# Optimization experiments

Measured on AMD Instinct MI355X. Metric: run time of the kernel, lower is better.

The kernel has to match this reference:

```python
import jax, jax.numpy as jnp
import numpy as np

B, H, L, D = 8, 8, 2048, 64  # head_sz = d_model // h = 512 // 8

def setup_inputs() -> dict:
    key = jax.random.key(0)
    kq, kk, kv = jax.random.split(key, 3)
    Q = jax.random.normal(kq, (B, H, L, D), dtype=jnp.float32)
    K = jax.random.normal(kk, (B, H, L, D), dtype=jnp.float32)
    V = jax.random.normal(kv, (B, H, L, D), dtype=jnp.float32)
    return {"Q": Q, "K": K, "V": V}

def reference(Q, K, V):
    head_sz = Q.shape[-1]
    # NOTE: original code divides by torch.tensor([head_sz]) (raw head size, not sqrt)
    prod = jnp.einsum('bhld,bhmd->bhlm', Q, K) / head_sz  # [B,H,L,L]
    att = jax.nn.softmax(prod, axis=-1)
    # dropout is identity in eval mode (reference is deterministic)
    res = jnp.einsum('bhlm,bhmd->bhld', att, V)  # [B,H,L,D]
    return (res, att)
```

## Files before the change

kernel.cpp:

```cpp
#include <hip/hip_runtime.h>

#define NB 8
#define NH 8
#define LSEQ 2048
#define DH 64

typedef __attribute__((ext_vector_type(8))) short bf16x8;
typedef __attribute__((ext_vector_type(4))) short bf16x4v;
typedef __attribute__((ext_vector_type(4))) float f32x4;

__device__ __forceinline__ short f2bf(float f) {
    union { float f; unsigned u; } v; v.f = f;
    unsigned r = v.u + 0x7fffu + ((v.u >> 16) & 1u);
    return (short)(r >> 16);
}
__device__ __forceinline__ float bf2f(short s) {
    union { unsigned u; float f; } v;
    v.u = ((unsigned)(unsigned short)s) << 16;
    return v.f;
}

__global__ __launch_bounds__(256, 2)
void sdpa_kernel(const float* __restrict__ Q, const float* __restrict__ K,
                 const float* __restrict__ V, float* __restrict__ out_res,
                 float* __restrict__ out_att)
{
    __shared__ short P[16 * 2048];

    const int tid  = threadIdx.x;
    const int lane = tid & 63;
    const int w    = tid >> 6;
    const int q16  = lane & 15;
    const int quad = lane >> 4;

    const int bh    = blockIdx.x >> 7;
    const int qbase = (blockIdx.x & 127) << 4;

    const size_t qkv0 = (size_t)bh * (LSEQ * DH);

    bf16x8 aq0, aq1;
    {
        const float* qp = Q + qkv0 + (size_t)(qbase + q16) * DH + quad * 8;
        float4 f0 = *(const float4*)(qp);
        float4 f1 = *(const float4*)(qp + 4);
        float4 f2 = *(const float4*)(qp + 32);
        float4 f3 = *(const float4*)(qp + 36);
        aq0[0]=f2bf(f0.x); aq0[1]=f2bf(f0.y); aq0[2]=f2bf(f0.z); aq0[3]=f2bf(f0.w);
        aq0[4]=f2bf(f1.x); aq0[5]=f2bf(f1.y); aq0[6]=f2bf(f1.z); aq0[7]=f2bf(f1.w);
        aq1[0]=f2bf(f2.x); aq1[1]=f2bf(f2.y); aq1[2]=f2bf(f2.z); aq1[3]=f2bf(f2.w);
        aq1[4]=f2bf(f3.x); aq1[5]=f2bf(f3.y); aq1[6]=f2bf(f3.z); aq1[7]=f2bf(f3.w);
    }

    const int key_lo = w << 9;
    for (int t = 0; t < 32; ++t) {
        const int key0 = key_lo + (t << 4);
        const float* kp = K + qkv0 + (size_t)(key0 + q16) * DH + quad * 8;
        float4 f0 = *(const float4*)(kp);
        float4 f1 = *(const float4*)(kp + 4);
        float4 f2 = *(const float4*)(kp + 32);
        float4 f3 = *(const float4*)(kp + 36);
        bf16x8 b0, b1;
        b0[0]=f2bf(f0.x); b0[1]=f2bf(f0.y); b0[2]=f2bf(f0.z); b0[3]=f2bf(f0.w);
        b0[4]=f2bf(f1.x); b0[5]=f2bf(f1.y); b0[6]=f2bf(f1.z); b0[7]=f2bf(f1.w);
        b1[0]=f2bf(f2.x); b1[1]=f2bf(f2.y); b1[2]=f2bf(f2.z); b1[3]=f2bf(f2.w);
        b1[4]=f2bf(f3.x); b1[5]=f2bf(f3.y); b1[6]=f2bf(f3.z); b1[7]=f2bf(f3.w);
        f32x4 acc = {0.f, 0.f, 0.f, 0.f};
        acc = __builtin_amdgcn_mfma_f32_16x16x32_bf16(aq0, b0, acc, 0, 0, 0);
        acc = __builtin_amdgcn_mfma_f32_16x16x32_bf16(aq1, b1, acc, 0, 0, 0);
        const int col = key0 + q16;
        const int chb = col >> 3;
        const int off = col & 7;
        #pragma unroll
        for (int r = 0; r < 4; ++r) {
            const int row = (quad << 2) + r;
            const float p = __expf(acc[r] * 0.015625f);
            P[(row << 11) + (((chb ^ (row & 7)) << 3) + off)] = f2bf(p);
        }
    }
    __syncthreads();

    float s = 0.f;
    {
        const int rb2 = q16 << 11;
        const int x7  = q16 & 7;
        for (int c = 0; c < 64; ++c) {
            const int ch = (quad << 6) + c;
            const bf16x8 v = *(const bf16x8*)&P[rb2 + ((ch ^ x7) << 3)];
            #pragma unroll
            for (int j = 0; j < 8; ++j) s += bf2f(v[j]);
        }
    }
    s += __shfl_xor(s, 16, 64);
    s += __shfl_xor(s, 32, 64);
    const float linv_own = 1.0f / s;

    const int nb = w << 4;
    const float* vb = V + qkv0 + nb + q16;
    f32x4 accA = {0.f,0.f,0.f,0.f}, accB = {0.f,0.f,0.f,0.f};
    const int rbq = q16 << 11;
    const int x7q = q16 & 7;
    for (int it = 0; it < 32; ++it) {
        const int chA = (it << 2) + quad;
        const int chB = chA + 128;
        const bf16x8 aA = *(const bf16x8*)&P[rbq + ((chA ^ x7q) << 3)];
        const bf16x8 aB = *(const bf16x8*)&P[rbq + ((chB ^ x7q) << 3)];
        const float* vpA = vb + (size_t)((it << 5) + (quad << 3)) * DH;
        const float* vpB = vpA + (size_t)1024 * DH;
        bf16x8 bA, bB;
        #pragma unroll
        for (int j = 0; j < 8; ++j) bA[j] = f2bf(vpA[(size_t)j * DH]);
        #pragma unroll
        for (int j = 0; j < 8; ++j) bB[j] = f2bf(vpB[(size_t)j * DH]);
        accA = __builtin_amdgcn_mfma_f32_16x16x32_bf16(aA, bA, accA, 0, 0, 0);
        accB = __builtin_amdgcn_mfma_f32_16x16x32_bf16(aB, bB, accB, 0, 0, 0);
    }
    {
        float* orow = out_res + qkv0 + (size_t)qbase * DH + nb + q16;
        #pragma unroll
        for (int r = 0; r < 4; ++r) {
            const int row = (quad << 2) + r;
            const float li = __shfl(linv_own, row, 64);
            orow[(size_t)row * DH] = (accA[r] + accB[r]) * li;
        }
    }

    float* ab = out_att + ((size_t)bh * LSEQ + qbase) * LSEQ;
    for (int i = 0; i < 32; ++i) {
        const int idx = tid + (i << 8);
        const int row = idx >> 9;
        const int col = (idx & 511) << 2;
        const int ch  = col >> 3;
        const int off = col & 7;
        const float li = __shfl(linv_own, row, 64);
        const bf16x4v v = *(const bf16x4v*)&P[(row << 11) + ((ch ^ (row & 7)) << 3) + off];
        float4 o;
        o.x = bf2f(v[0]) * li;
        o.y = bf2f(v[1]) * li;
        o.z = bf2f(v[2]) * li;
        o.w = bf2f(v[3]) * li;
        *(float4*)(ab + (size_t)row * LSEQ + col) = o;
    }
}

extern "C" void kernel_launch(void* const* d_in, const int* in_sizes, int n_in,
                              void* d_out, int out_size, void* d_ws, size_t ws_size,
                              hipStream_t stream) {
    const float* Q = (const float*)d_in[0];
    const float* K = (const float*)d_in[1];
    const float* V = (const float*)d_in[2];
    float* out_res = (float*)d_out;
    float* out_att = out_res + (size_t)NB * NH * LSEQ * DH;
    dim3 grid(NB * NH * (LSEQ / 16));
    sdpa_kernel<<<grid, dim3(256), 0, stream>>>(Q, K, V, out_res, out_att);
}
```

Before: 2.029 ms.

## Split into bf16 pre-conversion, row-sum pass, and streaming fused attention pass

Pre-converts K to bf16 and transposes V to bf16 in workspace. A separate pass recomputes QK^T and exp to get softmax row sums. The main kernel then recomputes scores, normalizes them, streams the attention matrix with nontemporal stores and does P@V through a small LDS staging buffer. This removes the large per-block LDS buffer that limited occupancy and the strided fp32 V gathers, at the cost of computing QK^T twice and launching extra kernels.

After: 1.666 ms. -17.9%, faster.

```diff
diff --git a/kernel.cpp b/kernel.cpp
--- a/kernel.cpp
+++ b/kernel.cpp
@@ -4,9 +4,9 @@
 #define NH 8
 #define LSEQ 2048
 #define DH 64
+#define NBH (NB * NH)
 
 typedef __attribute__((ext_vector_type(8))) short bf16x8;
-typedef __attribute__((ext_vector_type(4))) short bf16x4v;
 typedef __attribute__((ext_vector_type(4))) float f32x4;
 
 __device__ __forceinline__ short f2bf(float f) {
@@ -14,131 +14,180 @@
     unsigned r = v.u + 0x7fffu + ((v.u >> 16) & 1u);
     return (short)(r >> 16);
 }
-__device__ __forceinline__ float bf2f(short s) {
-    union { unsigned u; float f; } v;
-    v.u = ((unsigned)(unsigned short)s) << 16;
-    return v.f;
-}
-
-__global__ __launch_bounds__(256, 2)
-void sdpa_kernel(const float* __restrict__ Q, const float* __restrict__ K,
-                 const float* __restrict__ V, float* __restrict__ out_res,
-                 float* __restrict__ out_att)
-{
-    __shared__ short P[16 * 2048];
-
-    const int tid  = threadIdx.x;
+
+__device__ __forceinline__ void load_q_frags(const float* __restrict__ qp,
+                                             bf16x8& a0, bf16x8& a1) {
+    float4 f0 = *(const float4*)(qp);
+    float4 f1 = *(const float4*)(qp + 4);
+    float4 f2 = *(const float4*)(qp + 32);
+    float4 f3 = *(const float4*)(qp + 36);
+    a0[0]=f2bf(f0.x); a0[1]=f2bf(f0.y); a0[2]=f2bf(f0.z); a0[3]=f2bf(f0.w);
+    a0[4]=f2bf(f1.x); a0[5]=f2bf(f1.y); a0[6]=f2bf(f1.z); a0[7]=f2bf(f1.w);
+    a1[0]=f2bf(f2.x); a1[1]=f2bf(f2.y); a1[2]=f2bf(f2.z); a1[3]=f2bf(f2.w);
+    a1[4]=f2bf(f3.x); a1[5]=f2bf(f3.y); a1[6]=f2bf(f3.z); a1[7]=f2bf(f3.w);
+}
+
+__global__ __launch_bounds__(256)
+void conv_k(const float* __restrict__ K, short* __restrict__ Kbf) {
+    const size_t i = ((size_t)blockIdx.x * 256 + threadIdx.x) * 8;
+    float4 f0 = *(const float4*)(K + i);
+    float4 f1 = *(const float4*)(K + i + 4);
+    bf16x8 o;
+    o[0]=f2bf(f0.x); o[1]=f2bf(f0.y); o[2]=f2bf(f0.z); o[3]=f2bf(f0.w);
+    o[4]=f2bf(f1.x); o[5]=f2bf(f1.y); o[6]=f2bf(f1.z); o[7]=f2bf(f1.w);
+    *(bf16x8*)(Kbf + i) = o;
+}
+
+__global__ __launch_bounds__(256)
+void transp_v(const float* __restrict__ V, short* __restrict__ Vt) {
+    __shared__ __align__(16) short t[DH][64];
+    const int tid = threadIdx.x;
+    const int bh = blockIdx.x >> 5;
+    const int l0 = (blockIdx.x & 31) << 6;
+    const float* vb = V + ((size_t)bh * LSEQ + l0) * DH;
+    #pragma unroll
+    for (int p = 0; p < 4; ++p) {
+        const int l = (p << 4) + (tid >> 4);
+        const int d0 = (tid & 15) << 2;
+        float4 f = *(const float4*)(vb + (size_t)l * DH + d0);
+        const int lc = l >> 3, li = l & 7;
+        const int g = d0 >> 3;
+        t[d0 + 0][((lc ^ g) << 3) + li] = f2bf(f.x);
+        t[d0 + 1][((lc ^ g) << 3) + li] = f2bf(f.y);
+        t[d0 + 2][((lc ^ g) << 3) + li] = f2bf(f.z);
+        t[d0 + 3][((lc ^ g) << 3) + li] = f2bf(f.w);
+    }
+    __syncthreads();
+    const int d = tid >> 2;
+    const int s2 = (tid & 3) << 1;
+    const int g = d >> 3;
+    short* ob = Vt + ((size_t)bh * DH + d) * LSEQ + l0 + (s2 << 3);
+    *(bf16x8*)(ob)     = *(const bf16x8*)&t[d][(s2 ^ g) << 3];
+    *(bf16x8*)(ob + 8) = *(const bf16x8*)&t[d][((s2 + 1) ^ g) << 3];
+}
+
+__global__ __launch_bounds__(256, 4)
+void rowsum_k(const float* __restrict__ Q, const short* __restrict__ Kbf,
+              float* __restrict__ rsum) {
+    const int tid = threadIdx.x;
     const int lane = tid & 63;
-    const int w    = tid >> 6;
-    const int q16  = lane & 15;
+    const int w = tid >> 6;
+    const int q16 = lane & 15;
     const int quad = lane >> 4;
-
-    const int bh    = blockIdx.x >> 7;
-    const int qbase = (blockIdx.x & 127) << 4;
-
+    const int nb_ = ((blockIdx.x & 7) << 8) + (blockIdx.x >> 3);
+    const int bh = nb_ >> 5;
+    const int qbase = ((nb_ & 31) << 6) + (w << 4);
     const size_t qkv0 = (size_t)bh * (LSEQ * DH);
 
     bf16x8 aq0, aq1;
+    load_q_frags(Q + qkv0 + (size_t)(qbase + q16) * DH + quad * 8, aq0, aq1);
+
+    float rs0 = 0.f, rs1 = 0.f, rs2 = 0.f, rs3 = 0.f;
+    const short* kb = Kbf + qkv0 + (size_t)q16 * DH + quad * 8;
+    for (int c = 0; c < 64; ++c) {
+        const short* kp = kb + (size_t)(c << 5) * DH;
+        bf16x8 b00 = *(const bf16x8*)(kp);
+        bf16x8 b01 = *(const bf16x8*)(kp + 32);
+        bf16x8 b10 = *(const bf16x8*)(kp + 16 * DH);
+        bf16x8 b11 = *(const bf16x8*)(kp + 16 * DH + 32);
+        f32x4 s0 = {0.f,0.f,0.f,0.f}, s1 = {0.f,0.f,0.f,0.f};
+        s0 = __builtin_amdgcn_mfma_f32_16x16x32_bf16(aq0, b00, s0, 0, 0, 0);
+        s0 = __builtin_amdgcn_mfma_f32_16x16x32_bf16(aq1, b01, s0, 0, 0, 0);
+        s1 = __builtin_amdgcn_mfma_f32_16x16x32_bf16(aq0, b10, s1, 0, 0, 0);
+        s1 = __builtin_amdgcn_mfma_f32_16x16x32_bf16(aq1, b11, s1, 0, 0, 0);
+        rs0 += __expf(s0[0] * 0.015625f) + __expf(s1[0] * 0.015625f);
+        rs1 += __expf(s0[1] * 0.015625f) + __expf(s1[1] * 0.015625f);
+        rs2 += __expf(s0[2] * 0.015625f) + __expf(s1[2] * 0.015625f);
+        rs3 += __expf(s0[3] * 0.015625f) + __expf(s1[3] * 0.015625f);
+    }
+    #pragma unroll
+    for (int m = 1; m < 16; m <<= 1) {
+        rs0 += __shfl_xor(rs0, m, 64);
+        rs1 += __shfl_xor(rs1, m, 64);
+        rs2 += __shfl_xor(rs2, m, 64);
+        rs3 += __shfl_xor(rs3, m, 64);
+    }
+    if (q16 == 0) {
+        float* rp = rsum + (size_t)bh * LSEQ + qbase + (quad << 2);
+        rp[0] = rs0; rp[1] = rs1; rp[2] = rs2; rp[3] = rs3;
+    }
+}
+
+__global__ __launch_bounds__(256, 4)
+void sdpa_main(const float* __restrict__ Q, const short* __restrict__ Kbf,
+               const short* __restrict__ Vt, const float* __restrict__ rsum,
+               float* __restrict__ out_res, float* __restrict__ out_att) {
+    __shared__ __align__(16) short pbuf[4][16][40];
+    const int tid = threadIdx.x;
+    const int lane = tid & 63;
+    const int w = tid >> 6;
+    const int q16 = lane & 15;
+    const int quad = lane >> 4;
+
+    const int nb_ = ((blockIdx.x & 7) << 8) + (blockIdx.x >> 3);
+    const int bh = nb_ >> 5;
+    const int qbase = ((nb_ & 31) << 6) + (w << 4);
+    const size_t qkv0 = (size_t)bh * (LSEQ * DH);
+
+    bf16x8 aq0, aq1;
+    load_q_frags(Q + qkv0 + (size_t)(qbase + q16) * DH + quad * 8, aq0, aq1);
+
+    float linv[4];
     {
-        const float* qp = Q + qkv0 + (size_t)(qbase + q16) * DH + quad * 8;
-        float4 f0 = *(const float4*)(qp);
-        float4 f1 = *(const float4*)(qp + 4);
-        float4 f2 = *(const float4*)(qp + 32);
-        float4 f3 = *(const float4*)(qp + 36);
-        aq0[0]=f2bf(f0.x); aq0[1]=f2bf(f0.y); aq0[2]=f2bf(f0.z); aq0[3]=f2bf(f0.w);
-        aq0[4]=f2bf(f1.x); aq0[5]=f2bf(f1.y); aq0[6]=f2bf(f1.z); aq0[7]=f2bf(f1.w);
-        aq1[0]=f2bf(f2.x); aq1[1]=f2bf(f2.y); aq1[2]=f2bf(f2.z); aq1[3]=f2bf(f2.w);
-        aq1[4]=f2bf(f3.x); aq1[5]=f2bf(f3.y); aq1[6]=f2bf(f3.z); aq1[7]=f2bf(f3.w);
-    }
-
-    const int key_lo = w << 9;
-    for (int t = 0; t < 32; ++t) {
-        const int key0 = key_lo + (t << 4);
-        const float* kp = K + qkv0 + (size_t)(key0 + q16) * DH + quad * 8;
-        float4 f0 = *(const float4*)(kp);
-        float4 f1 = *(const float4*)(kp + 4);
-        float4 f2 = *(const float4*)(kp + 32);
-        float4 f3 = *(const float4*)(kp + 36);
-        bf16x8 b0, b1;
-        b0[0]=f2bf(f0.x); b0[1]=f2bf(f0.y); b0[2]=f2bf(f0.z); b0[3]=f2bf(f0.w);
-        b0[4]=f2bf(f1.x); b0[5]=f2bf(f1.y); b0[6]=f2bf(f1.z); b0[7]=f2bf(f1.w);
-        b1[0]=f2bf(f2.x); b1[1]=f2bf(f2.y); b1[2]=f2bf(f2.z); b1[3]=f2bf(f2.w);
-        b1[4]=f2bf(f3.x); b1[5]=f2bf(f3.y); b1[6]=f2bf(f3.z); b1[7]=f2bf(f3.w);
-        f32x4 acc = {0.f, 0.f, 0.f, 0.f};
-        acc = __builtin_amdgcn_mfma_f32_16x16x32_bf16(aq0, b0, acc, 0, 0, 0);
-        acc = __builtin_amdgcn_mfma_f32_16x16x32_bf16(aq1, b1, acc, 0, 0, 0);
-        const int col = key0 + q16;
-        const int chb = col >> 3;
-        const int off = col & 7;
+        const float* rp = rsum + (size_t)bh * LSEQ + qbase + (quad << 2);
+        linv[0] = 1.0f / rp[0];
+        linv[1] = 1.0f / rp[1];
+        linv[2] = 1.0f / rp[2];
+        linv[3] = 1.0f / rp[3];
+    }
+
+    f32x4 acc0 = {0.f,0.f,0.f,0.f}, acc1 = {0.f,0.f,0.f,0.f};
+    f32x4 acc2 = {0.f,0.f,0.f,0.f}, acc3 = {0.f,0.f,0.f,0.f};
+
+    const short* kb = Kbf + qkv0 + (size_t)q16 * DH + quad * 8;
+    const short* vb = Vt + (size_t)bh * (DH * LSEQ) + (size_t)q16 * LSEQ + quad * 8;
+    float* ab = out_att + ((size_t)bh * LSEQ + qbase + (quad << 2)) * LSEQ + q16;
+    short* pw = &pbuf[w][quad << 2][q16];
+    const short* pr = &pbuf[w][q16][quad << 3];
+
+    for (int c = 0; c < 64; ++c) {
+        const int col0 = c << 5;
+        const short* kp = kb + (size_t)col0 * DH;
+        bf16x8 b00 = *(const bf16x8*)(kp);
+        bf16x8 b01 = *(const bf16x8*)(kp + 32);
+        bf16x8 b10 = *(const bf16x8*)(kp + 16 * DH);
+        bf16x8 b11 = *(const bf16x8*)(kp + 16 * DH + 32);
+        f32x4 s0 = {0.f,0.f,0.f,0.f}, s1 = {0.f,0.f,0.f,0.f};
+        s0 = __builtin_amdgcn_mfma_f32_16x16x32_bf16(aq0, b00, s0, 0, 0, 0);
+        s0 = __builtin_amdgcn_mfma_f32_16x16x32_bf16(aq1, b01, s0, 0, 0, 0);
+        s1 = __builtin_amdgcn_mfma_f32_16x16x32_bf16(aq0, b10, s1, 0, 0, 0);
+        s1 = __builtin_amdgcn_mfma_f32_16x16x32_bf16(aq1, b11, s1, 0, 0, 0);
+
         #pragma unroll
         for (int r = 0; r < 4; ++r) {
-            const int row = (quad << 2) + r;
-            const float p = __expf(acc[r] * 0.015625f);
-            P[(row << 11) + (((chb ^ (row & 7)) << 3) + off)] = f2bf(p);
+            const float p0 = __expf(s0[r] * 0.015625f) * linv[r];
+            const float p1 = __expf(s1[r] * 0.015625f) * linv[r];
+            __builtin_nontemporal_store(p0, ab + (size_t)r * LSEQ + col0);
+            __builtin_nontemporal_store(p1, ab + (size_t)r * LSEQ + col0 + 16);
+            pw[r * 40]      = f2bf(p0);
+            pw[r * 40 + 16] = f2bf(p1);
         }
-    }
-    __syncthreads();
-
-    float s = 0.f;
-    {
-        const int rb2 = q16 << 11;
-        const int x7  = q16 & 7;
-        for (int c = 0; c < 64; ++c) {
-            const int ch = (quad << 6) + c;
-            const bf16x8 v = *(const bf16x8*)&P[rb2 + ((ch ^ x7) << 3)];
-            #pragma unroll
-            for (int j = 0; j < 8; ++j) s += bf2f(v[j]);
-        }
-    }
-    s += __shfl_xor(s, 16, 64);
-    s += __shfl_xor(s, 32, 64);
-    const float linv_own = 1.0f / s;
-
-    const int nb = w << 4;
-    const float* vb = V + qkv0 + nb + q16;
-    f32x4 accA = {0.f,0.f,0.f,0.f}, accB = {0.f,0.f,0.f,0.f};
-    const int rbq = q16 << 11;
-    const int x7q = q16 & 7;
-    for (int it = 0; it < 32; ++it) {
-        const int chA = (it << 2) + quad;
-        const int chB = chA + 128;
-        const bf16x8 aA = *(const bf16x8*)&P[rbq + ((chA ^ x7q) << 3)];
-        const bf16x8 aB = *(const bf16x8*)&P[rbq + ((chB ^ x7q) << 3)];
-        const float* vpA = vb + (size_t)((it << 5) + (quad << 3)) * DH;
-        const float* vpB = vpA + (size_t)1024 * DH;
-        bf16x8 bA, bB;
-        #pragma unroll
-        for (int j = 0; j < 8; ++j) bA[j] = f2bf(vpA[(size_t)j * DH]);
-        #pragma unroll
-        for (int j = 0; j < 8; ++j) bB[j] = f2bf(vpB[(size_t)j * DH]);
-        accA = __builtin_amdgcn_mfma_f32_16x16x32_bf16(aA, bA, accA, 0, 0, 0);
-        accB = __builtin_amdgcn_mfma_f32_16x16x32_bf16(aB, bB, accB, 0, 0, 0);
-    }
-    {
-        float* orow = out_res + qkv0 + (size_t)qbase * DH + nb + q16;
-        #pragma unroll
-        for (int r = 0; r < 4; ++r) {
-            const int row = (quad << 2) + r;
-            const float li = __shfl(linv_own, row, 64);
-            orow[(size_t)row * DH] = (accA[r] + accB[r]) * li;
-        }
-    }
-
-    float* ab = out_att + ((size_t)bh * LSEQ + qbase) * LSEQ;
-    for (int i = 0; i < 32; ++i) {
-        const int idx = tid + (i << 8);
-        const int row = idx >> 9;
-        const int col = (idx & 511) << 2;
-        const int ch  = col >> 3;
-        const int off = col & 7;
-        const float li = __shfl(linv_own, row, 64);
-        const bf16x4v v = *(const bf16x4v*)&P[(row << 11) + ((ch ^ (row & 7)) << 3) + off];
-        float4 o;
-        o.x = bf2f(v[0]) * li;
-        o.y = bf2f(v[1]) * li;
-        o.z = bf2f(v[2]) * li;
-        o.w = bf2f(v[3]) * li;
-        *(float4*)(ab + (size_t)row * LSEQ + col) = o;
+
+        const bf16x8 pa = *(const bf16x8*)pr;
+        const short* vp = vb + col0;
+        acc0 = __builtin_amdgcn_mfma_f32_16x16x32_bf16(pa, *(const bf16x8*)(vp),             acc0, 0, 0, 0);
+        acc1 = __builtin_amdgcn_mfma_f32_16x16x32_bf16(pa, *(const bf16x8*)(vp + 16 * LSEQ), acc1, 0, 0, 0);
+        acc2 = __builtin_amdgcn_mfma_f32_16x16x32_bf16(pa, *(const bf16x8*)(vp + 32 * LSEQ), acc2, 0, 0, 0);
+        acc3 = __builtin_amdgcn_mfma_f32_16x16x32_bf16(pa, *(const bf16x8*)(vp + 48 * LSEQ), acc3, 0, 0, 0);
+    }
+
+    float* rb = out_res + qkv0 + (size_t)(qbase + (quad << 2)) * DH + q16;
+    #pragma unroll
+    for (int r = 0; r < 4; ++r) {
+        __builtin_nontemporal_store(acc0[r], rb + (size_t)r * DH);
+        __builtin_nontemporal_store(acc1[r], rb + (size_t)r * DH + 16);
+        __builtin_nontemporal_store(acc2[r], rb + (size_t)r * DH + 32);
+        __builtin_nontemporal_store(acc3[r], rb + (size_t)r * DH + 48);
     }
 }
 
@@ -150,6 +199,13 @@
     const float* V = (const float*)d_in[2];
     float* out_res = (float*)d_out;
     float* out_att = out_res + (size_t)NB * NH * LSEQ * DH;
-    dim3 grid(NB * NH * (LSEQ / 16));
-    sdpa_kernel<<<grid, dim3(256), 0, stream>>>(Q, K, V, out_res, out_att);
-}
+
+    short* Kbf = (short*)d_ws;
+    short* Vt  = Kbf + (size_t)NBH * LSEQ * DH;
+    float* rsum = (float*)(Vt + (size_t)NBH * LSEQ * DH);
+
+    conv_k  <<<dim3(4096), dim3(256), 0, stream>>>(K, Kbf);
+    transp_v<<<dim3(2048), dim3(256), 0, stream>>>(V, Vt);
+    rowsum_k<<<dim3(2048), dim3(256), 0, stream>>>(Q, Kbf, rsum);
+    sdpa_main<<<dim3(2048), dim3(256), 0, stream>>>(Q, Kbf, Vt, rsum, out_res, out_att);
+}
```
